# Performance work log

Hardware: AMD Instinct MI355X
Metric: run time of the kernel (lower is better)

## Reference

```python
import jax, jax.numpy as jnp
import numpy as np

VOCAB = 100000
EMBED_DIM = 300
BATCH = 16384
N_CTX = 10
N_NEG = 20


def setup_inputs() -> dict:
    key = jax.random.key(0)
    k_ctx, k_cen, k_neg, k_w1, k_w2 = jax.random.split(key, 5)
    init_range = 0.5 / EMBED_DIM
    return {
        "context": jax.random.randint(k_ctx, (BATCH, N_CTX), 0, VOCAB),
        "center": jax.random.randint(k_cen, (BATCH,), 0, VOCAB),
        "negatives": jax.random.randint(k_neg, (BATCH, N_NEG), 0, VOCAB),
        "context_weight": jax.random.uniform(k_w1, (VOCAB, EMBED_DIM), jnp.float32, -init_range, init_range),
        "center_weight": jax.random.uniform(k_w2, (VOCAB, EMBED_DIM), jnp.float32, -init_range, init_range),
    }


def reference(context, center, negatives, context_weight, center_weight):
    # gather + mean over context words: [B, C, D] -> [B, D]
    ctx_mean = context_weight[context].mean(axis=1)
    center_emb = center_weight[center]            # [B, D]
    neg_emb = center_weight[negatives]            # [B, N, D]
    pos_score = jnp.sum(ctx_mean * center_emb, axis=1)          # [B]
    pos_loss = jax.nn.log_sigmoid(pos_score)                    # [B]
    neg_score = jnp.einsum("bnd,bd->bn", neg_emb, ctx_mean)    # [B, N]
    neg_loss = jax.nn.log_sigmoid(-neg_score).sum(axis=1)       # [B]
    return -(pos_loss + neg_loss).mean()
```

## Files before the change

### kernel.cpp

```cpp
#include <hip/hip_runtime.h>
#include <math.h>

#define BATCH 16384
#define N_CTX 10
#define N_NEG 20
#define DIM 300
#define WAVES_PER_BLOCK 4
#define NBLOCKS (BATCH / WAVES_PER_BLOCK)

__device__ __forceinline__ float wave_reduce_sum(float v) {
#pragma unroll
    for (int m = 32; m >= 1; m >>= 1)
        v += __shfl_xor(v, m, 64);
    return v;
}

__device__ __forceinline__ float log_sigmoid_f(float x) {
    float ax = fabsf(x);
    if (ax < 0.5f) {
        float x2 = x * x;
        return -0.6931471805599453f + 0.5f * x + x2 * (-0.125f + x2 * (1.0f / 192.0f));
    }
    return fminf(x, 0.0f) - log1pf(__expf(-ax));
}

__device__ __forceinline__ float dot4(float4 a, float4 b) {
    return a.x * b.x + a.y * b.y + a.z * b.z + a.w * b.w;
}

__global__ __launch_bounds__(256) void cbow_loss_kernel(
    const int* __restrict__ context,
    const int* __restrict__ center,
    const int* __restrict__ negatives,
    const float* __restrict__ ctx_w,
    const float* __restrict__ cen_w,
    float* __restrict__ partials)
{
    const int wave = threadIdx.x >> 6;
    const int lane = threadIdx.x & 63;
    const int b    = blockIdx.x * WAVES_PER_BLOCK + wave;

    int idx_ctx = 0, idx_cen = 0, idx_neg = 0;
    if (lane < N_CTX) idx_ctx = context[b * N_CTX + lane];
    if (lane == 0)    idx_cen = center[b];
    if (lane < N_NEG) idx_neg = negatives[b * N_NEG + lane];

    const bool has_tail = (lane < DIM - 256);
    const int  voff4    = lane * 4;
    const int  vofft    = 256 + lane;

    float4 ar[N_CTX]; float at[N_CTX];
#pragma unroll
    for (int j = 0; j < N_CTX; ++j) {
        int s = __builtin_amdgcn_readlane(idx_ctx, j);
        const float* rowp = ctx_w + (size_t)s * DIM;
        ar[j] = *(const float4*)(rowp + voff4);
        at[j] = has_tail ? rowp[vofft] : 0.0f;
    }

    {
        int s = __builtin_amdgcn_readlane(idx_cen, 0);
        const float* crow = cen_w + (size_t)s * DIM;
        float4 c4 = *(const float4*)(crow + voff4);
        float  ct = has_tail ? crow[vofft] : 0.0f;

        float4 nr[10]; float nt[10];
#pragma unroll
        for (int n = 0; n < 10; ++n) {
            int sn = __builtin_amdgcn_readlane(idx_neg, n);
            const float* rowp = cen_w + (size_t)sn * DIM;
            nr[n] = *(const float4*)(rowp + voff4);
            nt[n] = has_tail ? rowp[vofft] : 0.0f;
        }

        float4 m4 = make_float4(0.f, 0.f, 0.f, 0.f);
        float  mt = 0.f;
#pragma unroll
        for (int j = 0; j < N_CTX; ++j) {
            m4.x += ar[j].x; m4.y += ar[j].y; m4.z += ar[j].z; m4.w += ar[j].w;
            mt   += at[j];
        }
        m4.x *= 0.1f; m4.y *= 0.1f; m4.z *= 0.1f; m4.w *= 0.1f;
        mt *= 0.1f;

        float parts[N_NEG + 1];
        parts[N_NEG] = dot4(m4, c4) + mt * ct;
#pragma unroll
        for (int n = 0; n < 10; ++n)
            parts[n] = dot4(m4, nr[n]) + mt * nt[n];

#pragma unroll
        for (int n = 10; n < N_NEG; ++n) {
            int sn = __builtin_amdgcn_readlane(idx_neg, n);
            const float* rowp = cen_w + (size_t)sn * DIM;
            nr[n - 10] = *(const float4*)(rowp + voff4);
            nt[n - 10] = has_tail ? rowp[vofft] : 0.0f;
        }
#pragma unroll
        for (int n = 10; n < N_NEG; ++n)
            parts[n] = dot4(m4, nr[n - 10]) + mt * nt[n - 10];

        float pos = wave_reduce_sum(parts[N_NEG]);
        float loss = log_sigmoid_f(pos);
#pragma unroll
        for (int n = 0; n < N_NEG; ++n) {
            float ns = wave_reduce_sum(parts[n]);
            loss += log_sigmoid_f(-ns);
        }
        loss = -loss;

        __shared__ float s_loss[WAVES_PER_BLOCK];
        if (lane == 0) s_loss[wave] = loss;
        __syncthreads();
        if (threadIdx.x == 0)
            partials[blockIdx.x] = s_loss[0] + s_loss[1] + s_loss[2] + s_loss[3];
    }
}

__global__ __launch_bounds__(256) void reduce_partials_kernel(
    const float* __restrict__ partials, float* __restrict__ out)
{
    __shared__ double smem[256];
    double acc = 0.0;
    for (int i = threadIdx.x; i < NBLOCKS; i += 256) acc += (double)partials[i];
    smem[threadIdx.x] = acc;
    __syncthreads();
    for (int s = 128; s > 0; s >>= 1) {
        if ((int)threadIdx.x < s) smem[threadIdx.x] += smem[threadIdx.x + s];
        __syncthreads();
    }
    if (threadIdx.x == 0) out[0] = (float)(smem[0] * (1.0 / (double)BATCH));
}

extern "C" void kernel_launch(void* const* d_in, const int* in_sizes, int n_in,
                              void* d_out, int out_size, void* d_ws, size_t ws_size,
                              hipStream_t stream) {
    const int*   context   = (const int*)d_in[0];
    const int*   center    = (const int*)d_in[1];
    const int*   negatives = (const int*)d_in[2];
    const float* ctx_w     = (const float*)d_in[3];
    const float* cen_w     = (const float*)d_in[4];
    float*       out       = (float*)d_out;
    float*       partials  = (float*)d_ws;

    cbow_loss_kernel<<<NBLOCKS, 256, 0, stream>>>(
        context, center, negatives, ctx_w, cen_w, partials);
    reduce_partials_kernel<<<1, 256, 0, stream>>>(partials, out);
}
```

Before: 297.8 us.

## Process two batch elements per wave with software-pipelined row gathers

Each wave now handles two batch elements, issuing the gathers for the second element's rows before the first element's reductions and log-sigmoid math, so memory latency overlaps with compute. The 21 wave reductions are interleaved across butterfly stages instead of done one after another. Launch bounds ask for 3 blocks per SIMD, which caps register use. Register pressure rises and may cause spills, and half as many blocks are launched.

```diff
diff --git a/kernel.cpp b/kernel.cpp
--- a/kernel.cpp
+++ b/kernel.cpp
@@ -6,14 +6,8 @@
 #define N_NEG 20
 #define DIM 300
 #define WAVES_PER_BLOCK 4
-#define NBLOCKS (BATCH / WAVES_PER_BLOCK)
-
-__device__ __forceinline__ float wave_reduce_sum(float v) {
-#pragma unroll
-    for (int m = 32; m >= 1; m >>= 1)
-        v += __shfl_xor(v, m, 64);
-    return v;
-}
+#define ELEMS_PER_WAVE 2
+#define NBLOCKS (BATCH / (WAVES_PER_BLOCK * ELEMS_PER_WAVE))
 
 __device__ __forceinline__ float log_sigmoid_f(float x) {
     float ax = fabsf(x);
@@ -28,7 +22,7 @@
     return a.x * b.x + a.y * b.y + a.z * b.z + a.w * b.w;
 }
 
-__global__ __launch_bounds__(256) void cbow_loss_kernel(
+__global__ __launch_bounds__(256, 3) void cbow_loss_kernel(
     const int* __restrict__ context,
     const int* __restrict__ center,
     const int* __restrict__ negatives,
@@ -38,41 +32,43 @@
 {
     const int wave = threadIdx.x >> 6;
     const int lane = threadIdx.x & 63;
-    const int b    = blockIdx.x * WAVES_PER_BLOCK + wave;
+    const int e0   = (blockIdx.x * WAVES_PER_BLOCK + wave) * ELEMS_PER_WAVE;
 
-    int idx_ctx = 0, idx_cen = 0, idx_neg = 0;
-    if (lane < N_CTX) idx_ctx = context[b * N_CTX + lane];
-    if (lane == 0)    idx_cen = center[b];
-    if (lane < N_NEG) idx_neg = negatives[b * N_NEG + lane];
+    int ic0 = 0, in0 = 0, cen0 = 0, ic1 = 0, in1 = 0, cen1 = 0;
+    if (lane < N_CTX) { ic0 = context[e0 * N_CTX + lane];
+                        ic1 = context[(e0 + 1) * N_CTX + lane]; }
+    if (lane == 0)    { cen0 = center[e0];
+                        cen1 = center[e0 + 1]; }
+    if (lane < N_NEG) { in0 = negatives[e0 * N_NEG + lane];
+                        in1 = negatives[(e0 + 1) * N_NEG + lane]; }
 
     const bool has_tail = (lane < DIM - 256);
     const int  voff4    = lane * 4;
     const int  vofft    = 256 + lane;
 
+    auto load_row = [&](const float* __restrict__ w, int s, float4& r4, float& rt) {
+        const float* rowp = w + (size_t)s * DIM;
+        r4 = *(const float4*)(rowp + voff4);
+        rt = has_tail ? rowp[vofft] : 0.0f;
+    };
+
     float4 ar[N_CTX]; float at[N_CTX];
+    float4 nr[10];    float nt[10];
+    float4 nr2[10];   float nt2[10];
+    float4 c4;        float ct;
+    float parts[N_NEG + 1];
+
+    float wloss = 0.0f;
+
 #pragma unroll
-    for (int j = 0; j < N_CTX; ++j) {
-        int s = __builtin_amdgcn_readlane(idx_ctx, j);
-        const float* rowp = ctx_w + (size_t)s * DIM;
-        ar[j] = *(const float4*)(rowp + voff4);
-        at[j] = has_tail ? rowp[vofft] : 0.0f;
-    }
+    for (int j = 0; j < N_CTX; ++j)
+        load_row(ctx_w, __builtin_amdgcn_readlane(ic0, j), ar[j], at[j]);
+    load_row(cen_w, __builtin_amdgcn_readlane(cen0, 0), c4, ct);
+#pragma unroll
+    for (int n = 0; n < 10; ++n)
+        load_row(cen_w, __builtin_amdgcn_readlane(in0, n), nr[n], nt[n]);
 
     {
-        int s = __builtin_amdgcn_readlane(idx_cen, 0);
-        const float* crow = cen_w + (size_t)s * DIM;
-        float4 c4 = *(const float4*)(crow + voff4);
-        float  ct = has_tail ? crow[vofft] : 0.0f;
-
-        float4 nr[10]; float nt[10];
-#pragma unroll
-        for (int n = 0; n < 10; ++n) {
-            int sn = __builtin_amdgcn_readlane(idx_neg, n);
-            const float* rowp = cen_w + (size_t)sn * DIM;
-            nr[n] = *(const float4*)(rowp + voff4);
-            nt[n] = has_tail ? rowp[vofft] : 0.0f;
-        }
-
         float4 m4 = make_float4(0.f, 0.f, 0.f, 0.f);
         float  mt = 0.f;
 #pragma unroll
@@ -83,38 +79,86 @@
         m4.x *= 0.1f; m4.y *= 0.1f; m4.z *= 0.1f; m4.w *= 0.1f;
         mt *= 0.1f;
 
-        float parts[N_NEG + 1];
         parts[N_NEG] = dot4(m4, c4) + mt * ct;
+
+#pragma unroll
+        for (int n = 10; n < N_NEG; ++n)
+            load_row(cen_w, __builtin_amdgcn_readlane(in0, n), nr2[n - 10], nt2[n - 10]);
+
 #pragma unroll
         for (int n = 0; n < 10; ++n)
             parts[n] = dot4(m4, nr[n]) + mt * nt[n];
+#pragma unroll
+        for (int n = 10; n < N_NEG; ++n)
+            parts[n] = dot4(m4, nr2[n - 10]) + mt * nt2[n - 10];
+    }
 
 #pragma unroll
-        for (int n = 10; n < N_NEG; ++n) {
-            int sn = __builtin_amdgcn_readlane(idx_neg, n);
-            const float* rowp = cen_w + (size_t)sn * DIM;
-            nr[n - 10] = *(const float4*)(rowp + voff4);
-            nt[n - 10] = has_tail ? rowp[vofft] : 0.0f;
+    for (int j = 0; j < N_CTX; ++j)
+        load_row(ctx_w, __builtin_amdgcn_readlane(ic1, j), ar[j], at[j]);
+    load_row(cen_w, __builtin_amdgcn_readlane(cen1, 0), c4, ct);
+#pragma unroll
+    for (int n = 0; n < 10; ++n)
+        load_row(cen_w, __builtin_amdgcn_readlane(in1, n), nr[n], nt[n]);
+
+#pragma unroll
+    for (int m = 32; m >= 1; m >>= 1) {
+#pragma unroll
+        for (int n = 0; n <= N_NEG; ++n)
+            parts[n] += __shfl_xor(parts[n], m, 64);
+    }
+    {
+        float loss = log_sigmoid_f(parts[N_NEG]);
+#pragma unroll
+        for (int n = 0; n < N_NEG; ++n)
+            loss += log_sigmoid_f(-parts[n]);
+        wloss -= loss;
+    }
+
+    {
+        float4 m4 = make_float4(0.f, 0.f, 0.f, 0.f);
+        float  mt = 0.f;
+#pragma unroll
+        for (int j = 0; j < N_CTX; ++j) {
+            m4.x += ar[j].x; m4.y += ar[j].y; m4.z += ar[j].z; m4.w += ar[j].w;
+            mt   += at[j];
         }
+        m4.x *= 0.1f; m4.y *= 0.1f; m4.z *= 0.1f; m4.w *= 0.1f;
+        mt *= 0.1f;
+
+        parts[N_NEG] = dot4(m4, c4) + mt * ct;
+
 #pragma unroll
         for (int n = 10; n < N_NEG; ++n)
-            parts[n] = dot4(m4, nr[n - 10]) + mt * nt[n - 10];
+            load_row(cen_w, __builtin_amdgcn_readlane(in1, n), nr2[n - 10], nt2[n - 10]);
 
-        float pos = wave_reduce_sum(parts[N_NEG]);
-        float loss = log_sigmoid_f(pos);
 #pragma unroll
-        for (int n = 0; n < N_NEG; ++n) {
-            float ns = wave_reduce_sum(parts[n]);
-            loss += log_sigmoid_f(-ns);
-        }
-        loss = -loss;
+        for (int n = 0; n < 10; ++n)
+            parts[n] = dot4(m4, nr[n]) + mt * nt[n];
+#pragma unroll
+        for (int n = 10; n < N_NEG; ++n)
+            parts[n] = dot4(m4, nr2[n - 10]) + mt * nt2[n - 10];
+    }
 
-        __shared__ float s_loss[WAVES_PER_BLOCK];
-        if (lane == 0) s_loss[wave] = loss;
-        __syncthreads();
-        if (threadIdx.x == 0)
-            partials[blockIdx.x] = s_loss[0] + s_loss[1] + s_loss[2] + s_loss[3];
+#pragma unroll
+    for (int m = 32; m >= 1; m >>= 1) {
+#pragma unroll
+        for (int n = 0; n <= N_NEG; ++n)
+            parts[n] += __shfl_xor(parts[n], m, 64);
     }
+    {
+        float loss = log_sigmoid_f(parts[N_NEG]);
+#pragma unroll
+        for (int n = 0; n < N_NEG; ++n)
+            loss += log_sigmoid_f(-parts[n]);
+        wloss -= loss;
+    }
+
+    __shared__ float s_loss[WAVES_PER_BLOCK];
+    if (lane == 0) s_loss[wave] = wloss;
+    __syncthreads();
+    if (threadIdx.x == 0)
+        partials[blockIdx.x] = s_loss[0] + s_loss[1] + s_loss[2] + s_loss[3];
 }
 
 __global__ __launch_bounds__(256) void reduce_partials_kernel(
```

New measurement: 385.3 us. 29.4% more time.

## Process gathered rows in groups of five to cut registers and raise occupancy

Applied to the files above, without the earlier changes.

Rows are now loaded five at a time into one small register buffer, used for both context and negative embeddings, in place of holding ten context and ten negative rows at once. The cross-lane reductions for each group of five or six dot products are interleaved, so the shuffle chains run together and are not serialized one per score. Launch bounds ask for eight blocks per CU so more waves can hide gather latency. The cost is less memory-level parallelism inside each wave, with only five row loads in flight per group.

```diff
diff --git a/kernel.cpp b/kernel.cpp
--- a/kernel.cpp
+++ b/kernel.cpp
@@ -7,13 +7,6 @@
 #define DIM 300
 #define WAVES_PER_BLOCK 4
 #define NBLOCKS (BATCH / WAVES_PER_BLOCK)
-
-__device__ __forceinline__ float wave_reduce_sum(float v) {
-#pragma unroll
-    for (int m = 32; m >= 1; m >>= 1)
-        v += __shfl_xor(v, m, 64);
-    return v;
-}
 
 __device__ __forceinline__ float log_sigmoid_f(float x) {
     float ax = fabsf(x);
@@ -28,7 +21,7 @@
     return a.x * b.x + a.y * b.y + a.z * b.z + a.w * b.w;
 }
 
-__global__ __launch_bounds__(256) void cbow_loss_kernel(
+__global__ __launch_bounds__(256, 8) void cbow_loss_kernel(
     const int* __restrict__ context,
     const int* __restrict__ center,
     const int* __restrict__ negatives,
@@ -40,81 +33,99 @@
     const int lane = threadIdx.x & 63;
     const int b    = blockIdx.x * WAVES_PER_BLOCK + wave;
 
-    int idx_ctx = 0, idx_cen = 0, idx_neg = 0;
-    if (lane < N_CTX) idx_ctx = context[b * N_CTX + lane];
-    if (lane == 0)    idx_cen = center[b];
-    if (lane < N_NEG) idx_neg = negatives[b * N_NEG + lane];
+    int ic = 0, cenI = 0, inI = 0;
+    if (lane < N_CTX) ic   = context[b * N_CTX + lane];
+    if (lane == 0)    cenI = center[b];
+    if (lane < N_NEG) inI  = negatives[b * N_NEG + lane];
 
     const bool has_tail = (lane < DIM - 256);
     const int  voff4    = lane * 4;
     const int  vofft    = 256 + lane;
 
-    float4 ar[N_CTX]; float at[N_CTX];
+    float4 r4[5]; float rt[5];
+
+    auto load5 = [&](const float* __restrict__ w, int src, int base) {
 #pragma unroll
-    for (int j = 0; j < N_CTX; ++j) {
-        int s = __builtin_amdgcn_readlane(idx_ctx, j);
-        const float* rowp = ctx_w + (size_t)s * DIM;
-        ar[j] = *(const float4*)(rowp + voff4);
-        at[j] = has_tail ? rowp[vofft] : 0.0f;
+        for (int j = 0; j < 5; ++j) {
+            int s = __builtin_amdgcn_readlane(src, base + j);
+            const float* rowp = w + (size_t)s * DIM;
+            r4[j] = *(const float4*)(rowp + voff4);
+            rt[j] = has_tail ? rowp[vofft] : 0.0f;
+        }
+    };
+
+    float4 m4 = make_float4(0.f, 0.f, 0.f, 0.f);
+    float  mt = 0.f;
+    load5(ctx_w, ic, 0);
+#pragma unroll
+    for (int j = 0; j < 5; ++j) {
+        m4.x += r4[j].x; m4.y += r4[j].y; m4.z += r4[j].z; m4.w += r4[j].w;
+        mt   += rt[j];
+    }
+    load5(ctx_w, ic, 5);
+#pragma unroll
+    for (int j = 0; j < 5; ++j) {
+        m4.x += r4[j].x; m4.y += r4[j].y; m4.z += r4[j].z; m4.w += r4[j].w;
+        mt   += rt[j];
+    }
+    m4.x *= 0.1f; m4.y *= 0.1f; m4.z *= 0.1f; m4.w *= 0.1f;
+    mt *= 0.1f;
+
+    float acc;
+
+    {
+        float4 c4; float ct;
+        {
+            int s = __builtin_amdgcn_readlane(cenI, 0);
+            const float* crow = cen_w + (size_t)s * DIM;
+            c4 = *(const float4*)(crow + voff4);
+            ct = has_tail ? crow[vofft] : 0.0f;
+        }
+        load5(cen_w, inI, 0);
+
+        float p[6];
+        p[0] = dot4(m4, c4) + mt * ct;
+#pragma unroll
+        for (int j = 0; j < 5; ++j)
+            p[1 + j] = dot4(m4, r4[j]) + mt * rt[j];
+
+#pragma unroll
+        for (int m = 32; m >= 1; m >>= 1) {
+#pragma unroll
+            for (int k = 0; k < 6; ++k)
+                p[k] += __shfl_xor(p[k], m, 64);
+        }
+        acc = log_sigmoid_f(p[0]);
+#pragma unroll
+        for (int j = 0; j < 5; ++j)
+            acc += log_sigmoid_f(-p[1 + j]);
     }
 
-    {
-        int s = __builtin_amdgcn_readlane(idx_cen, 0);
-        const float* crow = cen_w + (size_t)s * DIM;
-        float4 c4 = *(const float4*)(crow + voff4);
-        float  ct = has_tail ? crow[vofft] : 0.0f;
-
-        float4 nr[10]; float nt[10];
 #pragma unroll
-        for (int n = 0; n < 10; ++n) {
-            int sn = __builtin_amdgcn_readlane(idx_neg, n);
-            const float* rowp = cen_w + (size_t)sn * DIM;
-            nr[n] = *(const float4*)(rowp + voff4);
-            nt[n] = has_tail ? rowp[vofft] : 0.0f;
-        }
-
-        float4 m4 = make_float4(0.f, 0.f, 0.f, 0.f);
-        float  mt = 0.f;
+    for (int g = 1; g < 4; ++g) {
+        load5(cen_w, inI, 5 * g);
+        float p[5];
 #pragma unroll
-        for (int j = 0; j < N_CTX; ++j) {
-            m4.x += ar[j].x; m4.y += ar[j].y; m4.z += ar[j].z; m4.w += ar[j].w;
-            mt   += at[j];
-        }
-        m4.x *= 0.1f; m4.y *= 0.1f; m4.z *= 0.1f; m4.w *= 0.1f;
-        mt *= 0.1f;
-
-        float parts[N_NEG + 1];
-        parts[N_NEG] = dot4(m4, c4) + mt * ct;
+        for (int j = 0; j < 5; ++j)
+            p[j] = dot4(m4, r4[j]) + mt * rt[j];
 #pragma unroll
-        for (int n = 0; n < 10; ++n)
-            parts[n] = dot4(m4, nr[n]) + mt * nt[n];
-
+        for (int m = 32; m >= 1; m >>= 1) {
 #pragma unroll
-        for (int n = 10; n < N_NEG; ++n) {
-            int sn = __builtin_amdgcn_readlane(idx_neg, n);
-            const float* rowp = cen_w + (size_t)sn * DIM;
-            nr[n - 10] = *(const float4*)(rowp + voff4);
-            nt[n - 10] = has_tail ? rowp[vofft] : 0.0f;
+            for (int k = 0; k < 5; ++k)
+                p[k] += __shfl_xor(p[k], m, 64);
         }
 #pragma unroll
-        for (int n = 10; n < N_NEG; ++n)
-            parts[n] = dot4(m4, nr[n - 10]) + mt * nt[n - 10];
+        for (int j = 0; j < 5; ++j)
+            acc += log_sigmoid_f(-p[j]);
+    }
 
-        float pos = wave_reduce_sum(parts[N_NEG]);
-        float loss = log_sigmoid_f(pos);
-#pragma unroll
-        for (int n = 0; n < N_NEG; ++n) {
-            float ns = wave_reduce_sum(parts[n]);
-            loss += log_sigmoid_f(-ns);
-        }
-        loss = -loss;
+    float wloss = -acc;
 
-        __shared__ float s_loss[WAVES_PER_BLOCK];
-        if (lane == 0) s_loss[wave] = loss;
-        __syncthreads();
-        if (threadIdx.x == 0)
-            partials[blockIdx.x] = s_loss[0] + s_loss[1] + s_loss[2] + s_loss[3];
-    }
+    __shared__ float s_loss[WAVES_PER_BLOCK];
+    if (lane == 0) s_loss[wave] = wloss;
+    __syncthreads();
+    if (threadIdx.x == 0)
+        partials[blockIdx.x] = s_loss[0] + s_loss[1] + s_loss[2] + s_loss[3];
 }
 
 __global__ __launch_bounds__(256) void reduce_partials_kernel(
```

Result: slower. 374.0 us (+25.6%).
